# Optimization experiments

Measured on AMD Instinct MI355X. Metric: run time of the kernel, lower is better.

The kernel has to match this reference:

```python
import jax, jax.numpy as jnp
import numpy as np


def log_g(x):
    # faithful to torch: where(x>=0, log(relu(x)+0.5), 5 - softplus(-x))
    return jnp.where(x >= 0, jnp.log(jax.nn.relu(x) + 0.5), 5.0 - jax.nn.softplus(-x))


def setup_inputs() -> dict:
    key = jax.random.key(0)
    ks = jax.random.split(key, 6)
    B, T, D, H = 8, 4096, 1024, 1024
    s = 1.0 / np.sqrt(D)
    return {
        "x": jax.random.normal(ks[0], (B, T, D), jnp.float32),
        "h_0": jax.random.normal(ks[1], (B, 1, H), jnp.float32),
        "Wz_w": jax.random.normal(ks[2], (D, H), jnp.float32) * s,
        "Wz_b": jax.random.normal(ks[3], (H,), jnp.float32) * 0.1,
        "Wh_w": jax.random.normal(ks[4], (D, H), jnp.float32) * s,
        "Wh_b": jax.random.normal(ks[5], (H,), jnp.float32) * 0.1,
    }


def reference(x, h_0, Wz_w, Wz_b, Wh_w, Wh_b):
    # k = W_z(x)
    k = jnp.einsum('btd,dh->bth', x, Wz_w) + Wz_b
    log_z = -jax.nn.softplus(-k)          # log sigmoid(k)
    log_coeffs = -jax.nn.softplus(k)      # log(1 - sigmoid(k))
    log_h0 = log_g(h_0)                                            # [B,1,H]
    log_tilde_h = log_g(jnp.einsum('btd,dh->bth', x, Wh_w) + Wh_b)  # [B,T,H]
    log_values = jnp.concatenate([log_h0, log_z + log_tilde_h], axis=1)  # [B,T+1,H]
    # a_star = pad(cumsum(log_coeffs, dim=1), (0,0,1,0)) -> one zero row at t=0
    a_star = jnp.pad(jnp.cumsum(log_coeffs, axis=1), ((0, 0), (1, 0), (0, 0)))  # [B,T+1,H]
    log_h = a_star + jax.lax.cumlogsumexp(log_values - a_star, axis=1)
    return jnp.exp(log_h)[:, 1:]  # [B,T,H]
```

## Files before the change

kernel.cpp:

```cpp
#include <hip/hip_runtime.h>
#include <hip/hip_bf16.h>
#include <stdint.h>

#define B_   8
#define T_   4096
#define D_   1024
#define H_   1024
#define M_   (B_ * T_)
#define NC_  64
#define TC_  64


typedef __attribute__((ext_vector_type(4))) float f32x4;
typedef __attribute__((ext_vector_type(8))) short bfr8;
typedef _Float16 f16;
typedef __attribute__((ext_vector_type(2))) _Float16 f16x2;

__device__ __forceinline__ unsigned short f2bf(float f) {
  unsigned int u = __float_as_uint(f);
  u += 0x7fffu + ((u >> 16) & 1u);
  return (unsigned short)(u >> 16);
}
__device__ __forceinline__ float bf2f(unsigned short h) {
  return __uint_as_float(((unsigned int)h) << 16);
}

__device__ __forceinline__ void gload16(const void* g, void* l) {
  __builtin_amdgcn_global_load_lds((const __attribute__((address_space(1))) void*)g,
                                   (__attribute__((address_space(3))) void*)l,
                                   16, 0, 0);
}

__device__ __forceinline__ float g_of(float hv) {
  return (hv >= 0.f) ? (hv + 0.5f)
                     : 148.4131591025766f / (1.f + __expf(-hv));
}

__global__ void prep_w(const float* __restrict__ Wz, const float* __restrict__ Wh,
                       unsigned short* __restrict__ wth, unsigned short* __restrict__ wtl,
                       float* __restrict__ whT, unsigned int* __restrict__ fcnt)
{
  if (blockIdx.x == 0 && blockIdx.y == 0 && threadIdx.x == 0) *fcnt = 0u;
  __shared__ float tile[32][33];
  int k0 = blockIdx.x * 32, n0 = blockIdx.y * 32;
  int tx = threadIdx.x & 31, ty = threadIdx.x >> 5;
  bool ish = (n0 >= 1024);
  const float* src = ish ? Wh : Wz;
  int nn0 = ish ? (n0 - 1024) : n0;
#pragma unroll
  for (int i = 0; i < 4; i++) {
    int k = k0 + ty * 4 + i;
    tile[ty * 4 + i][tx] = src[(size_t)k * 1024 + nn0 + tx];
  }
  __syncthreads();
#pragma unroll
  for (int i = 0; i < 4; i++) {
    int n = n0 + ty * 4 + i;
    float v = tile[tx][ty * 4 + i];
    unsigned short hi = f2bf(v);
    unsigned short lo = f2bf(v - bf2f(hi));
    wth[(size_t)n * 1024 + k0 + tx] = hi;
    wtl[(size_t)n * 1024 + k0 + tx] = lo;
    if (ish)
      whT[(size_t)(n - 1024) * 1024 + k0 + tx] = v;
  }
}

__global__ __launch_bounds__(256, 2) void gemm_cv(
    const float* __restrict__ x,
    const unsigned short* __restrict__ wth, const unsigned short* __restrict__ wtl,
    const float* __restrict__ bz, const float* __restrict__ bhb,
    f16x2* __restrict__ cvbuf,
    unsigned int* __restrict__ fcnt, unsigned int* __restrict__ flist,
    unsigned int fcap,
    float* __restrict__ Cc, float* __restrict__ Vv)
{
  __shared__ __align__(16) unsigned short As_h[4096], As_l[4096];
  __shared__ __align__(16) unsigned short Bzh[2048], Bzl[2048];
  __shared__ __align__(16) unsigned short Bhh[2048], Bhl[2048];
  int tid = threadIdx.x;
  int lane = tid & 63, wv = tid >> 6;
  int wr = wv >> 1, wc = wv & 1;
  int lrow = lane & 15, lhalf = lane >> 4;

  int bid = blockIdx.x;
  int cpx = gridDim.x >> 3;
  int swz = (bid & 7) * cpx + (bid >> 3);
  int grp = swz >> 7, wi = swz & 127;
  int mt = grp * 8 + (wi & 7);
  int nt = wi >> 3;
  int m0 = mt * 128, n0 = nt * 64;

  f32x4 accz[4][2], acch[4][2];
#pragma unroll
  for (int i = 0; i < 4; i++)
#pragma unroll
    for (int j = 0; j < 2; j++) {
      accz[i][j] = (f32x4){0.f, 0.f, 0.f, 0.f};
      acch[i][j] = (f32x4){0.f, 0.f, 0.f, 0.f};
    }

  int art = tid >> 3, ac4 = (tid & 7) * 4;
  int srow = tid >> 2, skb = (tid & 3) * 8;
  int blds = wv * 512;

  for (int k0 = 0; k0 < D_; k0 += 32) {
#pragma unroll
    for (int p = 0; p < 4; p++) {
      int row = p * 32 + art;
      uint4 vu = *(const uint4*)&x[(size_t)(m0 + row) * D_ + k0 + ac4];
      unsigned int hi01 = __builtin_amdgcn_perm(vu.y, vu.x, 0x07060302u);
      unsigned int hi23 = __builtin_amdgcn_perm(vu.w, vu.z, 0x07060302u);
      float l0 = __uint_as_float(vu.x) - __uint_as_float(vu.x & 0xffff0000u);
      float l1 = __uint_as_float(vu.y) - __uint_as_float(vu.y & 0xffff0000u);
      float l2 = __uint_as_float(vu.z) - __uint_as_float(vu.z & 0xffff0000u);
      float l3 = __uint_as_float(vu.w) - __uint_as_float(vu.w & 0xffff0000u);
      unsigned int lo01 = __builtin_amdgcn_perm(__float_as_uint(l1),
                                                __float_as_uint(l0), 0x07060302u);
      unsigned int lo23 = __builtin_amdgcn_perm(__float_as_uint(l3),
                                                __float_as_uint(l2), 0x07060302u);
      *(uint2*)&As_h[row * 32 + ac4] = make_uint2(hi01, hi23);
      *(uint2*)&As_l[row * 32 + ac4] = make_uint2(lo01, lo23);
    }
    {
      size_t gz = (size_t)(n0 + srow) * D_ + k0 + skb;
      size_t gh = (size_t)(1024 + n0 + srow) * D_ + k0 + skb;
      gload16(wth + gz, &Bzh[blds]);
      gload16(wtl + gz, &Bzl[blds]);
      gload16(wth + gh, &Bhh[blds]);
      gload16(wtl + gh, &Bhl[blds]);
    }
    __syncthreads();

    bfr8 ah[4], al[4], bzh[2], bzl[2], bhh[2], bhl[2];
    int ab = (wr * 64 + lrow) * 32 + lhalf * 8;
    int bb = (wc * 32 + lrow) * 32 + lhalf * 8;
#pragma unroll
    for (int f = 0; f < 4; f++) {
      ah[f] = *(const bfr8*)&As_h[ab + f * 512];
      al[f] = *(const bfr8*)&As_l[ab + f * 512];
    }
#pragma unroll
    for (int j = 0; j < 2; j++) {
      bzh[j] = *(const bfr8*)&Bzh[bb + j * 512];
      bzl[j] = *(const bfr8*)&Bzl[bb + j * 512];
      bhh[j] = *(const bfr8*)&Bhh[bb + j * 512];
      bhl[j] = *(const bfr8*)&Bhl[bb + j * 512];
    }
#pragma unroll
    for (int i = 0; i < 4; i++)
#pragma unroll
      for (int j = 0; j < 2; j++) {
        accz[i][j] = __builtin_amdgcn_mfma_f32_16x16x32_bf16(ah[i], bzh[j], accz[i][j], 0, 0, 0);
        accz[i][j] = __builtin_amdgcn_mfma_f32_16x16x32_bf16(al[i], bzh[j], accz[i][j], 0, 0, 0);
        accz[i][j] = __builtin_amdgcn_mfma_f32_16x16x32_bf16(ah[i], bzl[j], accz[i][j], 0, 0, 0);
        acch[i][j] = __builtin_amdgcn_mfma_f32_16x16x32_bf16(ah[i], bhh[j], acch[i][j], 0, 0, 0);
        acch[i][j] = __builtin_amdgcn_mfma_f32_16x16x32_bf16(al[i], bhh[j], acch[i][j], 0, 0, 0);
        acch[i][j] = __builtin_amdgcn_mfma_f32_16x16x32_bf16(ah[i], bhl[j], acch[i][j], 0, 0, 0);
      }
    __syncthreads();
  }

#pragma unroll
  for (int j = 0; j < 2; j++) {
    int col = n0 + wc * 32 + j * 16 + lrow;
    float kb = bz[col], hb = bhb[col];
    float CC = 1.f, VV = 0.f;
#pragma unroll
    for (int i = 0; i < 4; i++) {
      int row0 = m0 + wr * 64 + i * 16 + lhalf * 4;
      float SC = 1.f, SV = 0.f;
#pragma unroll
      for (int r = 0; r < 4; r++) {
        float kv = accz[i][j][r] + kb;
        float hv = acch[i][j][r] + hb;
        f16 kf = (f16)kv;
        float c  = 1.f / (1.f + __expf((float)kf));
        float v  = (1.f - c) * g_of(hv);
        size_t off = (size_t)(row0 + r) * H_ + col;
        f16x2 pr; pr[0] = kf; pr[1] = (f16)v;
        cvbuf[off] = pr;
        float vr = (float)pr[1];
        SV = fmaf(c, SV, vr);
        SC *= c;
        if (__builtin_fabsf(hv) < 1e-3f) {
          unsigned int p = atomicAdd(fcnt, 1u);
          if (p < fcap) flist[p] = (unsigned int)off;
        }
      }
      float oC = __shfl_xor(SC, 16);
      float oV = __shfl_xor(SV, 16);
      float nC = SC * oC;
      float nV = (lane & 16) ? fmaf(SC, oV, SV)
                             : fmaf(oC, SV, oV);
      oC = __shfl_xor(nC, 32);
      oV = __shfl_xor(nV, 32);
      float gC = nC * oC;
      float gV = (lane & 32) ? fmaf(nC, oV, nV)
                             : fmaf(oC, nV, oV);
      VV = fmaf(gC, VV, gV);
      CC *= gC;
    }
    if (lane < 16) {
      int bb2 = m0 >> 12;
      int ch  = ((m0 & 4095) >> 6) + wr;
      size_t oo = ((size_t)bb2 * NC_ + ch) * H_ + col;
      Cc[oo] = CC; Vv[oo] = VV;
    }
  }
}

__global__ void fixup_kc512(const float* __restrict__ x, const float* __restrict__ whT,
                            const float* __restrict__ bhb, f16x2* cvbuf,
                            const unsigned int* __restrict__ fcnt,
                            const unsigned int* __restrict__ flist, unsigned int fcap)
{
  unsigned int n = *fcnt; if (n > fcap) n = fcap;
  unsigned int gtid = blockIdx.x * blockDim.x + threadIdx.x;
  unsigned int nt = gridDim.x * blockDim.x;
  const unsigned int lim = (unsigned int)M_ * (unsigned int)H_;
  for (unsigned int i = gtid; i < n; i += nt) {
    unsigned int o = flist[i];
    if (o >= lim) continue;
    unsigned int row = o >> 10, col = o & 1023u;
    const float* xr = x + (size_t)row * D_;
    const float* wr = whT + (size_t)col * D_;
    float a1 = 0.f, a2 = 0.f;
    for (int d = 0; d < 512; d++)
      a1 = fmaf(xr[d], wr[d], a1);
    for (int d = 512; d < 1024; d++)
      a2 = fmaf(xr[d], wr[d], a2);
    float hs = (a1 + a2) + bhb[col];
    float g  = (hs >= 0.f) ? (hs + 0.5f)
                           : 148.4131591025766f / (1.f + __expf(-hs));
    f16x2 pr = cvbuf[o];
    float z  = 1.f / (1.f + __expf(-(float)pr[0]));
    pr[1] = (f16)(z * g);
    cvbuf[o] = pr;
  }
}

__global__ void scan_p1r(const f16x2* __restrict__ cv,
                         const unsigned int* __restrict__ fcnt,
                         const unsigned int* __restrict__ flist, unsigned int fcap,
                         float* __restrict__ Cc, float* __restrict__ Vv)
{
  unsigned int n = *fcnt; if (n > fcap) n = fcap;
  unsigned int gtid = blockIdx.x * blockDim.x + threadIdx.x;
  unsigned int nt = gridDim.x * blockDim.x;
  const unsigned int lim = (unsigned int)M_ * (unsigned int)H_;
  for (unsigned int idx = gtid; idx < n; idx += nt) {
    unsigned int o = flist[idx];
    if (o >= lim) continue;
    unsigned int row = o >> 10, col = o & 1023u;
    unsigned int b  = row >> 12;
    unsigned int ch = (row & 4095u) >> 6;
    size_t base = ((size_t)b * T_ + (size_t)ch * TC_) * H_ + col;
    float C = 1.f, V = 0.f;
    for (int i = 0; i < TC_; i++) {
      f16x2 p = cv[base + (size_t)i * H_];
      float c = 1.f / (1.f + __expf((float)p[0]));
      V = fmaf(c, V, (float)p[1]);
      C *= c;
    }
    size_t oo = ((size_t)b * NC_ + ch) * H_ + col;
    Cc[oo] = C; Vv[oo] = V;
  }
}

__global__ void scan_p2(const float* __restrict__ h0, const float* __restrict__ Cc,
                        const float* __restrict__ Vv, float* __restrict__ Hi)
{
  int idx = blockIdx.x * 256 + threadIdx.x;
  float hs = g_of(h0[idx]);
  int b = idx >> 10, h = idx & 1023;
  for (int ch = 0; ch < NC_; ch++) {
    size_t o = ((size_t)b * NC_ + ch) * H_ + h;
    Hi[o] = hs;
    hs = fmaf(Cc[o], hs, Vv[o]);
  }
}

__global__ void scan_p3(void* buf, const float* __restrict__ Hi)
{
  __shared__ f16x2 S[TC_][256];
  const f16x2* cv = (const f16x2*)buf;
  float* out = (float*)buf;
  int t = threadIdx.x;
  int hg = blockIdx.x, ch = blockIdx.y, b = blockIdx.z;
  int col = hg * 256 + t;
  size_t base = ((size_t)b * T_ + (size_t)ch * TC_) * H_ + col;
#pragma unroll 4
  for (int r = 0; r < TC_; r++)
    S[r][t] = cv[base + (size_t)r * H_];
  __syncthreads();
  float hs = Hi[((size_t)b * NC_ + ch) * H_ + col];
#pragma unroll 4
  for (int r = 0; r < TC_; r++) {
    f16x2 p = S[r][t];
    float c = 1.f / (1.f + __expf((float)p[0]));
    hs = fmaf(c, hs, (float)p[1]);
    out[base + (size_t)r * H_] = hs;
  }
}

extern "C" void kernel_launch(void* const* d_in, const int* in_sizes, int n_in,
                              void* d_out, int out_size, void* d_ws, size_t ws_size,
                              hipStream_t stream)
{
  const float* x  = (const float*)d_in[0];
  const float* h0 = (const float*)d_in[1];
  const float* Wz = (const float*)d_in[2];
  const float* bz = (const float*)d_in[3];
  const float* Wh = (const float*)d_in[4];
  const float* bh = (const float*)d_in[5];
  char* ws = (char*)d_ws;

  const size_t MiB = 1024u * 1024u;
  unsigned int* fcnt  = (unsigned int*)(ws);
  unsigned int* flist = (unsigned int*)(ws + 4096);
  const unsigned int fcap = 250u * 1024u;
  unsigned short* wth = (unsigned short*)(ws + 2 * MiB);
  unsigned short* wtl = (unsigned short*)(ws + 6 * MiB);
  float* Cc = (float*)(ws + 10 * MiB);
  float* Vv = (float*)(ws + 12 * MiB);
  float* Hi = (float*)(ws + 14 * MiB);
  float* whT = (float*)(ws + 16 * MiB);

  f16x2* cvbuf = (f16x2*)d_out;

  prep_w<<<dim3(32, 64), 256, 0, stream>>>(Wz, Wh, wth, wtl, whT, fcnt);
  gemm_cv<<<4096, 256, 0, stream>>>(x, wth, wtl, bz, bh, cvbuf, fcnt, flist, fcap, Cc, Vv);
  fixup_kc512<<<512, 256, 0, stream>>>(x, whT, bh, cvbuf, fcnt, flist, fcap);
  scan_p1r<<<256, 256, 0, stream>>>(cvbuf, fcnt, flist, fcap, Cc, Vv);
  scan_p2<<<32, 256, 0, stream>>>(h0, Cc, Vv, Hi);
  scan_p3<<<dim3(4, 64, 8), 256, 0, stream>>>(d_out, Hi);
}
```

Before: 684.9 us.

## Patch chunk carry linearly in fixup instead of rescanning flagged chunks

The GEMM epilogue now records, for each flagged near-zero element, the product of decay coefficients from that element to the end of its 64-step chunk. The fixup kernel uses this to atomically add the correction delta into the chunk's V aggregate. This removes the scan_p1r kernel, which rescanned 64 rows per flagged element. In exchange the epilogue does extra shuffles and suffix products, the fixup uses float atomics, and the flag-list capacity shrinks.

```diff
diff --git a/kernel.cpp b/kernel.cpp
--- a/kernel.cpp
+++ b/kernel.cpp
@@ -72,7 +72,7 @@
     const float* __restrict__ bz, const float* __restrict__ bhb,
     f16x2* __restrict__ cvbuf,
     unsigned int* __restrict__ fcnt, unsigned int* __restrict__ flist,
-    unsigned int fcap,
+    float* __restrict__ fsuf, unsigned int fcap,
     float* __restrict__ Cc, float* __restrict__ Vv)
 {
   __shared__ __align__(16) unsigned short As_h[4096], As_l[4096];
@@ -166,6 +166,7 @@
     int col = n0 + wc * 32 + j * 16 + lrow;
     float kb = bz[col], hb = bhb[col];
     float CC = 1.f, VV = 0.f;
+    float SCs[4], gCs[4];
 #pragma unroll
     for (int i = 0; i < 4; i++) {
       int row0 = m0 + wr * 64 + i * 16 + lhalf * 4;
@@ -183,10 +184,6 @@
         float vr = (float)pr[1];
         SV = fmaf(c, SV, vr);
         SC *= c;
-        if (__builtin_fabsf(hv) < 1e-3f) {
-          unsigned int p = atomicAdd(fcnt, 1u);
-          if (p < fcap) flist[p] = (unsigned int)off;
-        }
       }
       float oC = __shfl_xor(SC, 16);
       float oV = __shfl_xor(SV, 16);
@@ -200,6 +197,7 @@
                              : fmaf(oC, nV, oV);
       VV = fmaf(gC, VV, gV);
       CC *= gC;
+      SCs[i] = SC; gCs[i] = gC;
     }
     if (lane < 16) {
       int bb2 = m0 >> 12;
@@ -207,13 +205,52 @@
       size_t oo = ((size_t)bb2 * NC_ + ch) * H_ + col;
       Cc[oo] = CC; Vv[oo] = VV;
     }
+    float gsuf3 = 1.f;
+    float gsuf2 = gCs[3];
+    float gsuf1 = gCs[2] * gCs[3];
+    float gsuf0 = gCs[1] * gsuf1;
+    float gsuf[4] = {gsuf0, gsuf1, gsuf2, gsuf3};
+#pragma unroll
+    for (int i = 0; i < 4; i++) {
+      float a1 = __shfl(SCs[i], lrow + 16);
+      float a2 = __shfl(SCs[i], lrow + 32);
+      float a3 = __shfl(SCs[i], lrow + 48);
+      float lh = 1.f;
+      if (lhalf < 3) lh *= a3;
+      if (lhalf < 2) lh *= a2;
+      if (lhalf < 1) lh *= a1;
+      float base = lh * gsuf[i];
+      float cr[4], hv4[4];
+#pragma unroll
+      for (int r = 0; r < 4; r++) {
+        float kv = accz[i][j][r] + kb;
+        f16 kf = (f16)kv;
+        cr[r]  = 1.f / (1.f + __expf((float)kf));
+        hv4[r] = acch[i][j][r] + hb;
+      }
+      float rs1 = cr[2] * cr[3];
+      float rs[4] = {cr[1] * rs1, rs1, cr[3], 1.f};
+      int row0 = m0 + wr * 64 + i * 16 + lhalf * 4;
+#pragma unroll
+      for (int r = 0; r < 4; r++) {
+        if (__builtin_fabsf(hv4[r]) < 1e-3f) {
+          unsigned int p = atomicAdd(fcnt, 1u);
+          if (p < fcap) {
+            flist[p] = (unsigned int)((size_t)(row0 + r) * H_ + col);
+            fsuf[p]  = rs[r] * base;
+          }
+        }
+      }
+    }
   }
 }
 
 __global__ void fixup_kc512(const float* __restrict__ x, const float* __restrict__ whT,
                             const float* __restrict__ bhb, f16x2* cvbuf,
                             const unsigned int* __restrict__ fcnt,
-                            const unsigned int* __restrict__ flist, unsigned int fcap)
+                            const unsigned int* __restrict__ flist,
+                            const float* __restrict__ fsuf, unsigned int fcap,
+                            float* __restrict__ Vv)
 {
   unsigned int n = *fcnt; if (n > fcap) n = fcap;
   unsigned int gtid = blockIdx.x * blockDim.x + threadIdx.x;
@@ -235,36 +272,14 @@
                            : 148.4131591025766f / (1.f + __expf(-hs));
     f16x2 pr = cvbuf[o];
     float z  = 1.f / (1.f + __expf(-(float)pr[0]));
+    float vold = (float)pr[1];
     pr[1] = (f16)(z * g);
     cvbuf[o] = pr;
-  }
-}
-
-__global__ void scan_p1r(const f16x2* __restrict__ cv,
-                         const unsigned int* __restrict__ fcnt,
-                         const unsigned int* __restrict__ flist, unsigned int fcap,
-                         float* __restrict__ Cc, float* __restrict__ Vv)
-{
-  unsigned int n = *fcnt; if (n > fcap) n = fcap;
-  unsigned int gtid = blockIdx.x * blockDim.x + threadIdx.x;
-  unsigned int nt = gridDim.x * blockDim.x;
-  const unsigned int lim = (unsigned int)M_ * (unsigned int)H_;
-  for (unsigned int idx = gtid; idx < n; idx += nt) {
-    unsigned int o = flist[idx];
-    if (o >= lim) continue;
-    unsigned int row = o >> 10, col = o & 1023u;
-    unsigned int b  = row >> 12;
-    unsigned int ch = (row & 4095u) >> 6;
-    size_t base = ((size_t)b * T_ + (size_t)ch * TC_) * H_ + col;
-    float C = 1.f, V = 0.f;
-    for (int i = 0; i < TC_; i++) {
-      f16x2 p = cv[base + (size_t)i * H_];
-      float c = 1.f / (1.f + __expf((float)p[0]));
-      V = fmaf(c, V, (float)p[1]);
-      C *= c;
-    }
-    size_t oo = ((size_t)b * NC_ + ch) * H_ + col;
-    Cc[oo] = C; Vv[oo] = V;
+    float dv = (float)pr[1] - vold;
+    if (dv != 0.f) {
+      unsigned int b = row >> 12, ch = (row >> 6) & 63u;
+      atomicAdd(&Vv[((size_t)b * NC_ + ch) * H_ + col], fsuf[i] * dv);
+    }
   }
 }
 
@@ -319,7 +334,8 @@
   const size_t MiB = 1024u * 1024u;
   unsigned int* fcnt  = (unsigned int*)(ws);
   unsigned int* flist = (unsigned int*)(ws + 4096);
-  const unsigned int fcap = 250u * 1024u;
+  float*        fsuf  = (float*)(ws + 1 * MiB);
+  const unsigned int fcap = 192u * 1024u;
   unsigned short* wth = (unsigned short*)(ws + 2 * MiB);
   unsigned short* wtl = (unsigned short*)(ws + 6 * MiB);
   float* Cc = (float*)(ws + 10 * MiB);
@@ -330,9 +346,10 @@
   f16x2* cvbuf = (f16x2*)d_out;
 
   prep_w<<<dim3(32, 64), 256, 0, stream>>>(Wz, Wh, wth, wtl, whT, fcnt);
-  gemm_cv<<<4096, 256, 0, stream>>>(x, wth, wtl, bz, bh, cvbuf, fcnt, flist, fcap, Cc, Vv);
-  fixup_kc512<<<512, 256, 0, stream>>>(x, whT, bh, cvbuf, fcnt, flist, fcap);
-  scan_p1r<<<256, 256, 0, stream>>>(cvbuf, fcnt, flist, fcap, Cc, Vv);
+  gemm_cv<<<4096, 256, 0, stream>>>(x, wth, wtl, bz, bh, cvbuf,
+                                    fcnt, flist, fsuf, fcap, Cc, Vv);
+  fixup_kc512<<<512, 256, 0, stream>>>(x, whT, bh, cvbuf,
+                                       fcnt, flist, fsuf, fcap, Vv);
   scan_p2<<<32, 256, 0, stream>>>(h0, Cc, Vv, Hi);
   scan_p3<<<dim3(4, 64, 8), 256, 0, stream>>>(d_out, Hi);
 }
```

New measurement: 672.5 us. About the same (-1.8%).
